# Kernel optimization log

Hardware: AMD Instinct MI355X
Metric: run time of the kernel (lower is better)

## Reference

```python
import jax, jax.numpy as jnp
import numpy as np

D = 768  # hidden dim hard-coded in the module


def setup_inputs() -> dict:
    key = jax.random.key(0)
    k1, k2, k3, k4, k5 = jax.random.split(key, 5)
    N, M = 512, 512
    return {
        "text_output": jax.random.normal(k1, (N, D), dtype=jnp.float32),
        "visual_output": jax.random.normal(k2, (M, D), dtype=jnp.float32),
        "W1": jax.random.normal(k3, (D, D), dtype=jnp.float32),
        "W2": jax.random.normal(k4, (D, D), dtype=jnp.float32),
        "W3": jax.random.normal(k5, (D, D), dtype=jnp.float32),
    }


def reference(text_output, visual_output, W1, W2, W3):
    # C[n,m] = tanh( (text @ W1) . visual[m] )
    C = jnp.tanh((text_output @ W1) @ visual_output.T)            # (N, M)
    W2_text = text_output @ W2                                    # (N, D)
    W3_visual = visual_output @ W3.T                              # (M, D)
    # M[n,m,:] = tanh(W2_text[n] + W3_visual[m] * C[n,m])
    Mt = jnp.tanh(W2_text[:, None, :] + W3_visual[None, :, :] * C[..., None])  # (N, M, D)
    # score[n,m] = text[n] . M[n,m]  (replaces the per-row Python loop)
    score = jnp.einsum("nd,nmd->nm", text_output, Mt)             # (N, M)
    return score
```

## Files before the change

kernel.cpp:

```cpp
#include <hip/hip_runtime.h>

#define DD   768
#define NN   512
#define MM   512

#define PRE_K 2.88539008177792681472f

typedef _Float16 h8 __attribute__((ext_vector_type(8)));
typedef __attribute__((ext_vector_type(4))) float f32x4;

__device__ __forceinline__ float fexp(float x) { return __builtin_amdgcn_exp2f(x); }
__device__ __forceinline__ float frcp(float x) { return __builtin_amdgcn_rcpf(x); }
__device__ __forceinline__ float fast_tanh(float x) {
  return 1.0f - 2.0f * frcp(fexp(PRE_K * x) + 1.0f);
}

__device__ __forceinline__ void splitf(float x, ushort& h, ushort& l) {
  const _Float16 hh = (_Float16)x;
  const _Float16 ll = (_Float16)(x - (float)hh);
  h = __builtin_bit_cast(unsigned short, hh);
  l = __builtin_bit_cast(unsigned short, ll);
}

__global__ __launch_bounds__(256) void prep_kernel(
    const float* __restrict__ text, const float* __restrict__ visual,
    const float* __restrict__ W1, const float* __restrict__ W2,
    const float* __restrict__ W3,
    ushort* __restrict__ th, ushort* __restrict__ tl,
    ushort* __restrict__ vh, ushort* __restrict__ vl,
    ushort* __restrict__ w3h, ushort* __restrict__ w3l,
    ushort* __restrict__ w1th, ushort* __restrict__ w1tl,
    ushort* __restrict__ w2th, ushort* __restrict__ w2tl)
{
  __shared__ float Lt[32][33];
  const int b = blockIdx.x;
  const int t = threadIdx.x;

  if (b < 1344) {
    const float* src; ushort *dh, *dl; size_t off;
    if (b < 384)      { src = text;   dh = th;  dl = tl;  off = (size_t)b * 1024; }
    else if (b < 768) { src = visual; dh = vh;  dl = vl;  off = (size_t)(b - 384) * 1024; }
    else              { src = W3;     dh = w3h; dl = w3l; off = (size_t)(b - 768) * 1024; }
    const size_t i = off + (size_t)t * 4;
    const float4 v = *(const float4*)&src[i];
    ushort4 h, l;
    splitf(v.x, h.x, l.x); splitf(v.y, h.y, l.y);
    splitf(v.z, h.z, l.z); splitf(v.w, h.w, l.w);
    *(ushort4*)&dh[i] = h;
    *(ushort4*)&dl[i] = l;
  } else {
    const int tt = b - 1344;
    const bool second = tt >= 576;
    const int tile = second ? tt - 576 : tt;
    const float* W = second ? W2 : W1;
    ushort* oh = second ? w2th : w1th;
    ushort* ol = second ? w2tl : w1tl;
    const int k0 = (tile / 24) * 32, j0 = (tile % 24) * 32;
    {
      const int k = t >> 3, j4 = (t & 7) * 4;
      const float4 v = *(const float4*)&W[(size_t)(k0 + k) * DD + j0 + j4];
      Lt[j4 + 0][k] = v.x; Lt[j4 + 1][k] = v.y;
      Lt[j4 + 2][k] = v.z; Lt[j4 + 3][k] = v.w;
    }
    __syncthreads();
    {
      const int j = t >> 3, k4 = (t & 7) * 4;
      ushort4 h, l;
      splitf(Lt[j][k4 + 0], h.x, l.x); splitf(Lt[j][k4 + 1], h.y, l.y);
      splitf(Lt[j][k4 + 2], h.z, l.z); splitf(Lt[j][k4 + 3], h.w, l.w);
      *(ushort4*)&oh[(size_t)(j0 + j) * DD + k0 + k4] = h;
      *(ushort4*)&ol[(size_t)(j0 + j) * DD + k0 + k4] = l;
    }
  }
}

#define BK   32
#define LROW 40

template <bool ALO>
__device__ __forceinline__ void gemm_core(
    const ushort* __restrict__ Ahg, const ushort* __restrict__ Alg,
    const ushort* __restrict__ Bhg, const ushort* __restrict__ Blg,
    int i0, int j0, int k0, int nsteps, f32x4* acc)
{
  __shared__ ushort As[2][2][64 * LROW];
  __shared__ ushort Bs[2][2][64 * LROW];

  const int tid  = threadIdx.x;
  const int row  = tid >> 2;
  const int ks8  = (tid & 3) * 8;
  const size_t ga = (size_t)(i0 + row) * DD + k0 + ks8;
  const size_t gb = (size_t)(j0 + row) * DD + k0 + ks8;
  const int ldsw = row * LROW + ks8;

  const int lane = tid & 63, wave = tid >> 6;
  const int r15 = lane & 15, quad = lane >> 4;
  const int fa = (wave * 16 + r15) * LROW + quad * 8;
  const int fb = r15 * LROW + quad * 8;

  h8 pah = *(const h8*)(Ahg + ga);
  h8 pal; if (ALO) pal = *(const h8*)(Alg + ga);
  h8 pbh = *(const h8*)(Bhg + gb);
  h8 pbl = *(const h8*)(Blg + gb);

  int p = 0;
  *(h8*)&As[0][0][ldsw] = pah;
  if (ALO) *(h8*)&As[0][1][ldsw] = pal;
  *(h8*)&Bs[0][0][ldsw] = pbh; *(h8*)&Bs[0][1][ldsw] = pbl;
  __syncthreads();

  for (int s = 0; s < nsteps; ++s) {
    const bool more = (s + 1 < nsteps);
    if (more) {
      pah = *(const h8*)(Ahg + ga + (s + 1) * BK);
      if (ALO) pal = *(const h8*)(Alg + ga + (s + 1) * BK);
      pbh = *(const h8*)(Bhg + gb + (s + 1) * BK);
      pbl = *(const h8*)(Blg + gb + (s + 1) * BK);
    }
    const h8 a_h = *(const h8*)&As[p][0][fa];
    h8 a_l; if (ALO) a_l = *(const h8*)&As[p][1][fa];
    h8 b_h[4], b_l[4];
    #pragma unroll
    for (int c = 0; c < 4; ++c) {
      b_h[c] = *(const h8*)&Bs[p][0][fb + c * 16 * LROW];
      b_l[c] = *(const h8*)&Bs[p][1][fb + c * 16 * LROW];
    }
    #pragma unroll
    for (int c = 0; c < 4; ++c)
      acc[c] = __builtin_amdgcn_mfma_f32_16x16x32_f16(a_h, b_h[c], acc[c], 0, 0, 0);
    #pragma unroll
    for (int c = 0; c < 4; ++c)
      acc[c] = __builtin_amdgcn_mfma_f32_16x16x32_f16(a_h, b_l[c], acc[c], 0, 0, 0);
    if (ALO) {
      #pragma unroll
      for (int c = 0; c < 4; ++c)
        acc[c] = __builtin_amdgcn_mfma_f32_16x16x32_f16(a_l, b_h[c], acc[c], 0, 0, 0);
    }
    if (more) {
      const int q = p ^ 1;
      *(h8*)&As[q][0][ldsw] = pah;
      if (ALO) *(h8*)&As[q][1][ldsw] = pal;
      *(h8*)&Bs[q][0][ldsw] = pbh; *(h8*)&Bs[q][1][ldsw] = pbl;
    }
    __syncthreads();
    p ^= 1;
  }
}

__global__ __launch_bounds__(256) void mfma1_kernel(
    const ushort* __restrict__ th, const ushort* __restrict__ tl,
    const ushort* __restrict__ vh, const ushort* __restrict__ vl,
    const ushort* __restrict__ w1th, const ushort* __restrict__ w1tl,
    const ushort* __restrict__ w2th, const ushort* __restrict__ w2tl,
    const ushort* __restrict__ w3h, const ushort* __restrict__ w3l,
    ushort* __restrict__ Ah, ushort* __restrict__ Al,
    float* __restrict__ kw2t, float* __restrict__ kw3v)
{
  const int z  = blockIdx.z;
  const int j0 = blockIdx.x * 64;
  const int i0 = blockIdx.y * 64;

  f32x4 acc[4];
  #pragma unroll
  for (int c = 0; c < 4; ++c) acc[c] = (f32x4){0.f, 0.f, 0.f, 0.f};

  if (z == 0)
    gemm_core<true >(th, tl, w1th, w1tl, i0, j0, 0, DD / BK, acc);
  else if (z == 1)
    gemm_core<false>(th, tl, w2th, w2tl, i0, j0, 0, DD / BK, acc);
  else
    gemm_core<false>(vh, vl, w3h,  w3l,  i0, j0, 0, DD / BK, acc);

  const int lane = threadIdx.x & 63, wave = threadIdx.x >> 6;
  const int r15 = lane & 15, quad = lane >> 4;
  if (z == 0) {
    #pragma unroll
    for (int c = 0; c < 4; ++c)
      #pragma unroll
      for (int r = 0; r < 4; ++r) {
        const size_t o = (size_t)(i0 + wave * 16 + quad * 4 + r) * DD + j0 + c * 16 + r15;
        splitf(acc[c][r], Ah[o], Al[o]);
      }
  } else {
    float* Out = (z == 1) ? kw2t : kw3v;
    #pragma unroll
    for (int c = 0; c < 4; ++c)
      #pragma unroll
      for (int r = 0; r < 4; ++r)
        Out[(size_t)(i0 + wave * 16 + quad * 4 + r) * DD + j0 + c * 16 + r15] =
            acc[c][r] * PRE_K;
  }
}

__global__ __launch_bounds__(256) void mfma2_kernel(
    const ushort* __restrict__ Ah, const ushort* __restrict__ Al,
    const ushort* __restrict__ vh, const ushort* __restrict__ vl,
    float* __restrict__ Q)
{
  const int z  = blockIdx.z;
  const int j0 = blockIdx.x * 64;
  const int i0 = blockIdx.y * 64;

  f32x4 acc[4];
  #pragma unroll
  for (int c = 0; c < 4; ++c) acc[c] = (f32x4){0.f, 0.f, 0.f, 0.f};
  gemm_core<true>(Ah, Al, vh, vl, i0, j0, z * (DD / 4), (DD / 4) / BK, acc);

  const int lane = threadIdx.x & 63, wave = threadIdx.x >> 6;
  const int r15 = lane & 15, quad = lane >> 4;
  float* Out = Q + (size_t)z * NN * MM;
  #pragma unroll
  for (int c = 0; c < 4; ++c)
    #pragma unroll
    for (int r = 0; r < 4; ++r)
      Out[(size_t)(i0 + wave * 16 + quad * 4 + r) * MM + j0 + c * 16 + r15] = acc[c][r];
}

#define DCH    64
#define DRANGE 256
#define MLDW   68

__global__ __launch_bounds__(256) void main_kernel(
    const float* __restrict__ text, const float* __restrict__ kw2t,
    const float* __restrict__ kw3v, const float* __restrict__ Q,
    float* __restrict__ Spart)
{
  __shared__ float sbuf[2][64 * MLDW];

  const int tid = threadIdx.x;
  const int nl = tid >> 4;
  const int ml = tid & 15;
  const int n0 = blockIdx.y * 16;
  const int m0 = blockIdx.x * 32;
  const int z  = blockIdx.z;
  const int n  = n0 + nl;
  const int mA = m0 + ml, mB = mA + 16;
  const int dbase = z * DRANGE;

  float cA = 0.f, cB = 0.f;
  #pragma unroll
  for (int zz = 0; zz < 4; ++zz) {
    const float* q = Q + (size_t)zz * NN * MM + (size_t)n * MM;
    cA += q[mA]; cB += q[mB];
  }
  cA = fast_tanh(cA); cB = fast_tanh(cB);

  float4 aA = {0.f, 0.f, 0.f, 0.f};
  float4 aB = {0.f, 0.f, 0.f, 0.f};

  const int srow = tid >> 4;
  const int sc4  = (tid & 15) << 2;
  const float* gt  = &text[(size_t)(n0 + srow) * DD + dbase + sc4];
  const float* g2  = &kw2t[(size_t)(n0 + srow) * DD + dbase + sc4];
  const float* g3a = &kw3v[(size_t)(m0 + srow) * DD + dbase + sc4];
  const float* g3b = &kw3v[(size_t)(m0 + 16 + srow) * DD + dbase + sc4];
  const int wt  = srow * MLDW + sc4;
  const int w2  = (16 + srow) * MLDW + sc4;
  const int w3a = (32 + srow) * MLDW + sc4;
  const int w3b = (48 + srow) * MLDW + sc4;

  float4 rt  = *(const float4*)gt;
  float4 r2  = *(const float4*)g2;
  float4 r3a = *(const float4*)g3a;
  float4 r3b = *(const float4*)g3b;
  int p = 0;
  *(float4*)&sbuf[0][wt]  = rt;
  *(float4*)&sbuf[0][w2]  = r2;
  *(float4*)&sbuf[0][w3a] = r3a;
  *(float4*)&sbuf[0][w3b] = r3b;
  __syncthreads();

  #pragma unroll
  for (int c = 0; c < DRANGE / DCH; ++c) {
    const bool more = (c + 1 < DRANGE / DCH);
    if (more) {
      rt  = *(const float4*)(gt  + (c + 1) * DCH);
      r2  = *(const float4*)(g2  + (c + 1) * DCH);
      r3a = *(const float4*)(g3a + (c + 1) * DCH);
      r3b = *(const float4*)(g3b + (c + 1) * DCH);
    }
    const float* bp = sbuf[p];
    #pragma unroll 4
    for (int j = 0; j < DCH; j += 4) {
      const float4 tv  = *(const float4*)&bp[nl * MLDW + j];
      const float4 w2v = *(const float4*)&bp[(16 + nl) * MLDW + j];
      const float4 w3A = *(const float4*)&bp[(32 + ml) * MLDW + j];
      const float4 w3B = *(const float4*)&bp[(48 + ml) * MLDW + j];
      aA.x = fmaf(tv.x, frcp(fexp(fmaf(w3A.x, cA, w2v.x)) + 1.0f), aA.x);
      aA.y = fmaf(tv.y, frcp(fexp(fmaf(w3A.y, cA, w2v.y)) + 1.0f), aA.y);
      aA.z = fmaf(tv.z, frcp(fexp(fmaf(w3A.z, cA, w2v.z)) + 1.0f), aA.z);
      aA.w = fmaf(tv.w, frcp(fexp(fmaf(w3A.w, cA, w2v.w)) + 1.0f), aA.w);
      aB.x = fmaf(tv.x, frcp(fexp(fmaf(w3B.x, cB, w2v.x)) + 1.0f), aB.x);
      aB.y = fmaf(tv.y, frcp(fexp(fmaf(w3B.y, cB, w2v.y)) + 1.0f), aB.y);
      aB.z = fmaf(tv.z, frcp(fexp(fmaf(w3B.z, cB, w2v.z)) + 1.0f), aB.z);
      aB.w = fmaf(tv.w, frcp(fexp(fmaf(w3B.w, cB, w2v.w)) + 1.0f), aB.w);
    }
    if (more) {
      const int q = p ^ 1;
      *(float4*)&sbuf[q][wt]  = rt;
      *(float4*)&sbuf[q][w2]  = r2;
      *(float4*)&sbuf[q][w3a] = r3a;
      *(float4*)&sbuf[q][w3b] = r3b;
    }
    __syncthreads();
    p ^= 1;
  }

  float* Sp = Spart + (size_t)z * NN * MM + (size_t)n * MM;
  Sp[mA] = (aA.x + aA.y) + (aA.z + aA.w);
  Sp[mB] = (aB.x + aB.y) + (aB.z + aB.w);
}

__global__ __launch_bounds__(256) void combine_kernel(
    const float* __restrict__ Spart, const float* __restrict__ text,
    float* __restrict__ out)
{
  __shared__ float red[256];
  __shared__ float Tsh[2];
  const int b = blockIdx.x, t = threadIdx.x;
  const int n0 = b * 2;
  const int half = t >> 7;
  const int lt = t & 127;

  const float* tr = text + (size_t)(n0 + half) * DD;
  float s = 0.f;
  #pragma unroll
  for (int i = 0; i < DD / 128; ++i) s += tr[lt + i * 128];
  red[t] = s;
  __syncthreads();
  #pragma unroll
  for (int st = 64; st > 0; st >>= 1) {
    if (lt < st) red[t] += red[t + st];
    __syncthreads();
  }
  if (lt == 0) Tsh[half] = red[t];
  __syncthreads();

  const size_t i = (size_t)b * 1024 + (size_t)t * 4;
  const size_t S = (size_t)NN * MM;
  const float Tn = Tsh[half];
  const float4 s0 = *(const float4*)&Spart[i];
  const float4 s1 = *(const float4*)&Spart[S + i];
  const float4 s2 = *(const float4*)&Spart[2 * S + i];
  float4 o;
  o.x = Tn - 2.0f * (s0.x + s1.x + s2.x);
  o.y = Tn - 2.0f * (s0.y + s1.y + s2.y);
  o.z = Tn - 2.0f * (s0.z + s1.z + s2.z);
  o.w = Tn - 2.0f * (s0.w + s1.w + s2.w);
  *(float4*)&out[i] = o;
}

extern "C" void kernel_launch(void* const* d_in, const int* in_sizes, int n_in,
                              void* d_out, int out_size, void* d_ws, size_t ws_size,
                              hipStream_t stream) {
  const float* text   = (const float*)d_in[0];
  const float* visual = (const float*)d_in[1];
  const float* W1     = (const float*)d_in[2];
  const float* W2     = (const float*)d_in[3];
  const float* W3     = (const float*)d_in[4];
  float* out = (float*)d_out;

  char* base = (char*)d_ws;
  ushort* th   = (ushort*)(base);
  ushort* tl   = (ushort*)(base + 786432);
  ushort* vh   = (ushort*)(base + 1572864);
  ushort* vl   = (ushort*)(base + 2359296);
  ushort* w1th = (ushort*)(base + 3145728);
  ushort* w1tl = (ushort*)(base + 4325376);
  ushort* w2th = (ushort*)(base + 5505024);
  ushort* w2tl = (ushort*)(base + 6684672);
  ushort* w3h  = (ushort*)(base + 7864320);
  ushort* w3l  = (ushort*)(base + 9043968);
  ushort* Ah   = (ushort*)(base + 10223616);
  ushort* Al   = (ushort*)(base + 11010048);
  float*  kw2t = (float*) (base + 11796480);
  float*  kw3v = (float*) (base + 13369344);
  float*  Q     = (float*)(base + 3145728);
  float*  Spart = (float*)(base + 7864320);

  hipLaunchKernelGGL(prep_kernel, dim3(2496), dim3(256), 0, stream,
                     text, visual, W1, W2, W3,
                     th, tl, vh, vl, w3h, w3l, w1th, w1tl, w2th, w2tl);
  hipLaunchKernelGGL(mfma1_kernel, dim3(DD / 64, NN / 64, 3), dim3(256), 0, stream,
                     th, tl, vh, vl, w1th, w1tl, w2th, w2tl, w3h, w3l,
                     Ah, Al, kw2t, kw3v);
  hipLaunchKernelGGL(mfma2_kernel, dim3(MM / 64, NN / 64, 4), dim3(256), 0, stream,
                     Ah, Al, vh, vl, Q);
  hipLaunchKernelGGL(main_kernel, dim3(MM / 32, NN / 16, 3), dim3(256), 0, stream,
                     text, kw2t, kw3v, Q, Spart);
  hipLaunchKernelGGL(combine_kernel, dim3(NN * MM / 1024), dim3(256), 0, stream,
                     Spart, text, out);
}
```

Before: 137.8 us.

## Replace combine kernel with atomic accumulation into pre-initialized output

Removes the separate combine kernel and the Spart partial buffers. The prep kernel gains 256 extra blocks that compute each text row sum and write it into the output as the initial value. main_kernel then atomically adds -2 times its d-range partial directly into the output. This drops one launch and the write and re-read of three NxM partial arrays, at the cost of three float atomics per output element and a summation order that is no longer deterministic.

```diff
diff --git a/kernel.cpp b/kernel.cpp
--- a/kernel.cpp
+++ b/kernel.cpp
@@ -30,7 +30,8 @@
     ushort* __restrict__ vh, ushort* __restrict__ vl,
     ushort* __restrict__ w3h, ushort* __restrict__ w3l,
     ushort* __restrict__ w1th, ushort* __restrict__ w1tl,
-    ushort* __restrict__ w2th, ushort* __restrict__ w2tl)
+    ushort* __restrict__ w2th, ushort* __restrict__ w2tl,
+    float* __restrict__ out)
 {
   __shared__ float Lt[32][33];
   const int b = blockIdx.x;
@@ -48,7 +49,7 @@
     splitf(v.z, h.z, l.z); splitf(v.w, h.w, l.w);
     *(ushort4*)&dh[i] = h;
     *(ushort4*)&dl[i] = l;
-  } else {
+  } else if (b < 2496) {
     const int tt = b - 1344;
     const bool second = tt >= 576;
     const int tile = second ? tt - 576 : tt;
@@ -71,6 +72,27 @@
       *(ushort4*)&oh[(size_t)(j0 + j) * DD + k0 + k4] = h;
       *(ushort4*)&ol[(size_t)(j0 + j) * DD + k0 + k4] = l;
     }
+  } else {
+    float* red = (float*)Lt;
+    const int u = b - 2496;
+    const int n0 = u * 2;
+    const int half = t >> 7;
+    const int lt = t & 127;
+
+    const float* tr = text + (size_t)(n0 + half) * DD;
+    float s = 0.f;
+    #pragma unroll
+    for (int i = 0; i < DD / 128; ++i) s += tr[lt + i * 128];
+    red[t] = s;
+    __syncthreads();
+    #pragma unroll
+    for (int st = 64; st > 0; st >>= 1) {
+      if (lt < st) red[t] += red[t + st];
+      __syncthreads();
+    }
+    const float Tn = red[half << 7];
+    float4 o; o.x = Tn; o.y = Tn; o.z = Tn; o.w = Tn;
+    *(float4*)&out[(size_t)(n0 + half) * MM + lt * 4] = o;
   }
 }
 
@@ -223,7 +245,7 @@
 __global__ __launch_bounds__(256) void main_kernel(
     const float* __restrict__ text, const float* __restrict__ kw2t,
     const float* __restrict__ kw3v, const float* __restrict__ Q,
-    float* __restrict__ Spart)
+    float* __restrict__ out)
 {
   __shared__ float sbuf[2][64 * MLDW];
 
@@ -306,48 +328,9 @@
     p ^= 1;
   }
 
-  float* Sp = Spart + (size_t)z * NN * MM + (size_t)n * MM;
-  Sp[mA] = (aA.x + aA.y) + (aA.z + aA.w);
-  Sp[mB] = (aB.x + aB.y) + (aB.z + aB.w);
-}
-
-__global__ __launch_bounds__(256) void combine_kernel(
-    const float* __restrict__ Spart, const float* __restrict__ text,
-    float* __restrict__ out)
-{
-  __shared__ float red[256];
-  __shared__ float Tsh[2];
-  const int b = blockIdx.x, t = threadIdx.x;
-  const int n0 = b * 2;
-  const int half = t >> 7;
-  const int lt = t & 127;
-
-  const float* tr = text + (size_t)(n0 + half) * DD;
-  float s = 0.f;
-  #pragma unroll
-  for (int i = 0; i < DD / 128; ++i) s += tr[lt + i * 128];
-  red[t] = s;
-  __syncthreads();
-  #pragma unroll
-  for (int st = 64; st > 0; st >>= 1) {
-    if (lt < st) red[t] += red[t + st];
-    __syncthreads();
-  }
-  if (lt == 0) Tsh[half] = red[t];
-  __syncthreads();
-
-  const size_t i = (size_t)b * 1024 + (size_t)t * 4;
-  const size_t S = (size_t)NN * MM;
-  const float Tn = Tsh[half];
-  const float4 s0 = *(const float4*)&Spart[i];
-  const float4 s1 = *(const float4*)&Spart[S + i];
-  const float4 s2 = *(const float4*)&Spart[2 * S + i];
-  float4 o;
-  o.x = Tn - 2.0f * (s0.x + s1.x + s2.x);
-  o.y = Tn - 2.0f * (s0.y + s1.y + s2.y);
-  o.z = Tn - 2.0f * (s0.z + s1.z + s2.z);
-  o.w = Tn - 2.0f * (s0.w + s1.w + s2.w);
-  *(float4*)&out[i] = o;
+  float* op = out + (size_t)n * MM;
+  unsafeAtomicAdd(&op[mA], -2.0f * ((aA.x + aA.y) + (aA.z + aA.w)));
+  unsafeAtomicAdd(&op[mB], -2.0f * ((aB.x + aB.y) + (aB.z + aB.w)));
 }
 
 extern "C" void kernel_launch(void* const* d_in, const int* in_sizes, int n_in,
@@ -375,19 +358,16 @@
   ushort* Al   = (ushort*)(base + 11010048);
   float*  kw2t = (float*) (base + 11796480);
   float*  kw3v = (float*) (base + 13369344);
-  float*  Q     = (float*)(base + 3145728);
-  float*  Spart = (float*)(base + 7864320);
-
-  hipLaunchKernelGGL(prep_kernel, dim3(2496), dim3(256), 0, stream,
+  float*  Q    = (float*) (base + 3145728);
+
+  hipLaunchKernelGGL(prep_kernel, dim3(2752), dim3(256), 0, stream,
                      text, visual, W1, W2, W3,
-                     th, tl, vh, vl, w3h, w3l, w1th, w1tl, w2th, w2tl);
+                     th, tl, vh, vl, w3h, w3l, w1th, w1tl, w2th, w2tl, out);
   hipLaunchKernelGGL(mfma1_kernel, dim3(DD / 64, NN / 64, 3), dim3(256), 0, stream,
                      th, tl, vh, vl, w1th, w1tl, w2th, w2tl, w3h, w3l,
                      Ah, Al, kw2t, kw3v);
   hipLaunchKernelGGL(mfma2_kernel, dim3(MM / 64, NN / 64, 4), dim3(256), 0, stream,
                      Ah, Al, vh, vl, Q);
   hipLaunchKernelGGL(main_kernel, dim3(MM / 32, NN / 16, 3), dim3(256), 0, stream,
-                     text, kw2t, kw3v, Q, Spart);
-  hipLaunchKernelGGL(combine_kernel, dim3(NN * MM / 1024), dim3(256), 0, stream,
-                     Spart, text, out);
-}
+                     text, kw2t, kw3v, Q, out);
+}
```

Measured after the change: 135.3 us. No clear change (-1.8%).
